# Kernel tuning notes

Measured on AMD Instinct MI355X. Metric: run time of the kernel, lower is better.

Reference implementation:

```python
import jax, jax.numpy as jnp
import numpy as np

N_SHOTS, N_SAMPLES, IMG = 10, 192, 256
M = N_SHOTS * N_SAMPLES  # 1920 k-space samples


def _radial_traj():
    # mri-nufft initialize_2D_radial: uniform spoke angles over pi,
    # radii in [-0.5, 0.5) with N_SAMPLES points per spoke.
    r = (np.arange(N_SAMPLES) - N_SAMPLES / 2) / N_SAMPLES
    ang = np.pi * np.arange(N_SHOTS) / N_SHOTS
    kx = np.cos(ang)[:, None] * r[None, :]
    ky = np.sin(ang)[:, None] * r[None, :]
    return np.stack([kx, ky], axis=-1).reshape(-1, 2).astype(np.float32)


def _phase_mats(samples):
    # Separable NDFT phase factors: exp(-2i*pi*k_x*i), exp(-2i*pi*k_y*j)
    grid = jnp.arange(IMG, dtype=jnp.float32) - IMG / 2  # centered pixel coords
    Ax = jnp.exp(-2j * jnp.pi * samples[:, 0:1] * grid[None, :]).astype(jnp.complex64)  # (M, IMG)
    Ay = jnp.exp(-2j * jnp.pi * samples[:, 1:2] * grid[None, :]).astype(jnp.complex64)  # (M, IMG)
    return Ax, Ay


def _pipe_density(samples, n_iter=10):
    # Pipe & Menon density compensation: w <- w / |F F^H w| (density=True in gpunufft).
    Ax, Ay = _phase_mats(samples)
    w = jnp.ones(M, jnp.complex64)
    for _ in range(n_iter):
        t = Ax.conj() * w[:, None]                    # (M, IMG)
        img = jnp.einsum('mi,mj->ij', t, Ay.conj())   # F^H w, (IMG, IMG)
        back = jnp.einsum('mi,ij,mj->m', Ax, img, Ay) # F F^H w, (M,)
        w = w / jnp.maximum(jnp.abs(back), 1e-12).astype(jnp.complex64)
    return jnp.abs(w).astype(jnp.float32)


def setup_inputs() -> dict:
    key = jax.random.key(0)
    k1, k2 = jax.random.split(key)
    B, C = 64, 1
    x_real = jax.random.normal(k1, (B, C, IMG, IMG), dtype=jnp.float32)
    x_imag = jax.random.normal(k2, (B, C, IMG, IMG), dtype=jnp.float32)
    samples = jnp.asarray(_radial_traj())
    density = _pipe_density(samples)
    return {"x_real": x_real, "x_imag": x_imag, "samples": samples, "density": density}


def reference(x_real, x_imag, samples, density):
    x = (x_real + 1j * x_imag).astype(jnp.complex64)  # (B, C, IMG, IMG)
    Ax, Ay = _phase_mats(samples)
    # Forward NUFFT (type-2 NDFT): kspace[b,c,m] = sum_ij Ax[m,i] Ay[m,j] x[b,c,i,j]
    t = jnp.einsum('mi,bcij->bcmj', Ax, x)            # (B, C, M, IMG)
    kspace = jnp.einsum('mj,bcmj->bcm', Ay, t)        # (B, C, M)
    # Density-compensated adjoint NUFFT (type-1 NDFT)
    kw = kspace * density.astype(jnp.complex64)
    u = jnp.einsum('mi,bcm->bcmi', Ax.conj(), kw)     # (B, C, M, IMG)
    adj = jnp.einsum('mj,bcmi->bcij', Ay.conj(), u) / (IMG * IMG)
    return jnp.stack([adj.real, adj.imag], axis=-1)   # (B, C, IMG, IMG, 2)
```

## Files before the change

### kernel.cpp

```cpp
#include <hip/hip_runtime.h>
#include <hip/hip_bf16.h>
#include <hip/hip_fp16.h>

constexpr int IMG_ = 256;
constexpr int M_   = 1920;
constexpr int B_   = 64;
constexpr int MI_  = M_ * IMG_;
constexpr int IMG2 = IMG_ * IMG_;

typedef _Float16 half8 __attribute__((ext_vector_type(8)));
typedef float    floatx4 __attribute__((ext_vector_type(4)));

__global__ __launch_bounds__(256) void phase1_k(
    const float* __restrict__ samples,
    _Float16* __restrict__ axh_r, _Float16* __restrict__ axh_i,
    _Float16* __restrict__ ayh_r, _Float16* __restrict__ ayh_i) {
  int idx = blockIdx.x * 256 + threadIdx.x;
  if (idx >= MI_) return;
  int m = idx >> 8;
  int i = idx & 255;
  float g  = (float)i - 128.0f;
  float kx = samples[2 * m + 0];
  float ky = samples[2 * m + 1];
  float sx, cx, sy, cy;
  sincospif(-2.0f * kx * g, &sx, &cx);
  sincospif(-2.0f * ky * g, &sy, &cy);
  axh_r[idx] = (_Float16)cx; axh_i[idx] = (_Float16)sx;
  ayh_r[idx] = (_Float16)cy; ayh_i[idx] = (_Float16)sy;
}

__global__ __launch_bounds__(256) void phase2_k(
    const float* __restrict__ samples,
    _Float16* __restrict__ axtc_r, _Float16* __restrict__ axtc_i,
    _Float16* __restrict__ aytc_r, _Float16* __restrict__ aytc_i) {
  int m = blockIdx.x * 256 + threadIdx.x;
  if (m >= M_) return;
  int i = blockIdx.y;
  float g  = (float)i - 128.0f;
  float kx = samples[2 * m + 0];
  float ky = samples[2 * m + 1];
  float sx, cx, sy, cy;
  sincospif(-2.0f * kx * g, &sx, &cx);
  sincospif(-2.0f * ky * g, &sy, &cy);
  int o = i * M_ + m;
  axtc_r[o] = (_Float16)cx; axtc_i[o] = (_Float16)(-sx);
  aytc_r[o] = (_Float16)cy; aytc_i[o] = (_Float16)(-sy);
}

__global__ __launch_bounds__(256) void xt_k(
    const float* __restrict__ xr, const float* __restrict__ xi,
    _Float16* __restrict__ xth_r, _Float16* __restrict__ xth_i) {
  __shared__ float tr[32][33], ti[32][33];
  const int t = threadIdx.x;
  const int b = blockIdx.z;
  const int i0 = blockIdx.x * 32, j0 = blockIdx.y * 32;
  const int r = t >> 5, c = t & 31;
#pragma unroll
  for (int k = 0; k < 4; ++k) {
    int row = r + k * 8;
    tr[row][c] = xr[(size_t)b * IMG2 + (i0 + row) * IMG_ + j0 + c];
    ti[row][c] = xi[(size_t)b * IMG2 + (i0 + row) * IMG_ + j0 + c];
  }
  __syncthreads();
#pragma unroll
  for (int k = 0; k < 4; ++k) {
    int row = r + k * 8;
    xth_r[(size_t)b * IMG2 + (j0 + row) * IMG_ + i0 + c] = (_Float16)tr[c][row];
    xth_i[(size_t)b * IMG2 + (j0 + row) * IMG_ + i0 + c] = (_Float16)ti[c][row];
  }
}

__global__ __launch_bounds__(256) void fwd_k(
    const _Float16* __restrict__ axh_r, const _Float16* __restrict__ axh_i,
    const _Float16* __restrict__ ayh_r, const _Float16* __restrict__ ayh_i,
    const _Float16* __restrict__ xth_r, const _Float16* __restrict__ xth_i,
    const float* __restrict__ density,
    _Float16* __restrict__ kwh_r, _Float16* __restrict__ kwh_i) {
  __shared__ _Float16 asr[64 * 40], asi[64 * 40];
  __shared__ _Float16 bsr[64 * 40], bsi[64 * 40];

  const int t = threadIdx.x;
  const int w = t >> 6;
  const int l = t & 63;
  const int lr = l & 15;
  const int q  = l >> 4;
  const int b  = blockIdx.y;
  const int m0 = blockIdx.x * 64;
  const _Float16* __restrict__ xrb = xth_r + (size_t)b * IMG2;
  const _Float16* __restrict__ xib = xth_i + (size_t)b * IMG2;

  float kr[4] = {0.f, 0.f, 0.f, 0.f};
  float ki[4] = {0.f, 0.f, 0.f, 0.f};
  const floatx4 z4 = {0.f, 0.f, 0.f, 0.f};

  for (int jc = 0; jc < 4; ++jc) {
    const int j0 = jc * 64;
    floatx4 accr[4] = {z4, z4, z4, z4};
    floatx4 acci[4] = {z4, z4, z4, z4};

    for (int kt = 0; kt < 8; ++kt) {
      const int i0 = kt * 32;
      __syncthreads();
#pragma unroll
      for (int p = 0; p < 2; ++p) {
        int slot = t + p * 256;
        int row = slot >> 3, seg = slot & 7;
        *(uint2*)&asr[row * 40 + seg * 4] = *(const uint2*)&axh_r[(m0 + row) * IMG_ + i0 + seg * 4];
        *(uint2*)&asi[row * 40 + seg * 4] = *(const uint2*)&axh_i[(m0 + row) * IMG_ + i0 + seg * 4];
        *(uint2*)&bsr[row * 40 + seg * 4] = *(const uint2*)&xrb[(j0 + row) * IMG_ + i0 + seg * 4];
        *(uint2*)&bsi[row * 40 + seg * 4] = *(const uint2*)&xib[(j0 + row) * IMG_ + i0 + seg * 4];
      }
      __syncthreads();

      half8 ar = *(const half8*)&asr[(w * 16 + lr) * 40 + q * 8];
      half8 ai = *(const half8*)&asi[(w * 16 + lr) * 40 + q * 8];
      half8 nai = -ai;
#pragma unroll
      for (int jt = 0; jt < 4; ++jt) {
        half8 br = *(const half8*)&bsr[(jt * 16 + lr) * 40 + q * 8];
        half8 bi = *(const half8*)&bsi[(jt * 16 + lr) * 40 + q * 8];
        accr[jt] = __builtin_amdgcn_mfma_f32_16x16x32_f16(ar,  br, accr[jt], 0, 0, 0);
        accr[jt] = __builtin_amdgcn_mfma_f32_16x16x32_f16(nai, bi, accr[jt], 0, 0, 0);
        acci[jt] = __builtin_amdgcn_mfma_f32_16x16x32_f16(ar,  bi, acci[jt], 0, 0, 0);
        acci[jt] = __builtin_amdgcn_mfma_f32_16x16x32_f16(ai,  br, acci[jt], 0, 0, 0);
      }
    }

#pragma unroll
    for (int jt = 0; jt < 4; ++jt) {
      int j = j0 + jt * 16 + lr;
#pragma unroll
      for (int reg = 0; reg < 4; ++reg) {
        int m = m0 + w * 16 + q * 4 + reg;
        float yr = (float)ayh_r[m * IMG_ + j];
        float yi = (float)ayh_i[m * IMG_ + j];
        float tr = accr[jt][reg], ti = acci[jt][reg];
        kr[reg] = fmaf(yr, tr, fmaf(-yi, ti, kr[reg]));
        ki[reg] = fmaf(yr, ti, fmaf(yi, tr, ki[reg]));
      }
    }
  }

#pragma unroll
  for (int reg = 0; reg < 4; ++reg) {
#pragma unroll
    for (int off = 1; off < 16; off <<= 1) {
      kr[reg] += __shfl_xor(kr[reg], off);
      ki[reg] += __shfl_xor(ki[reg], off);
    }
  }
  if (lr == 0) {
#pragma unroll
    for (int reg = 0; reg < 4; ++reg) {
      int m = m0 + w * 16 + q * 4 + reg;
      float d = density[m];
      kwh_r[b * M_ + m] = (_Float16)(kr[reg] * d);
      kwh_i[b * M_ + m] = (_Float16)(ki[reg] * d);
    }
  }
}

__global__ __launch_bounds__(256) void adj_k(
    const _Float16* __restrict__ axtc_r, const _Float16* __restrict__ axtc_i,
    const _Float16* __restrict__ aytc_r, const _Float16* __restrict__ aytc_i,
    const _Float16* __restrict__ kwh_r, const _Float16* __restrict__ kwh_i,
    float* __restrict__ out) {
  __shared__ _Float16 asr[64 * 40], asi[64 * 40];
  __shared__ _Float16 wsr[64 * 40], wsi[64 * 40];

  const int t = threadIdx.x;
  const int w = t >> 6;
  const int l = t & 63;
  const int lr = l & 15;
  const int q  = l >> 4;
  const int b  = blockIdx.z;
  const int i0 = blockIdx.x * 64;
  const int j0 = blockIdx.y * 64;

  const floatx4 z4 = {0.f, 0.f, 0.f, 0.f};
  floatx4 accr[4] = {z4, z4, z4, z4};
  floatx4 acci[4] = {z4, z4, z4, z4};

  for (int mt = 0; mt < M_ / 32; ++mt) {
    const int m0 = mt * 32;
    __syncthreads();
#pragma unroll
    for (int p = 0; p < 2; ++p) {
      int slot = t + p * 256;
      int row = slot >> 3, seg = slot & 7;
      *(uint2*)&asr[row * 40 + seg * 4] = *(const uint2*)&axtc_r[(i0 + row) * M_ + m0 + seg * 4];
      *(uint2*)&asi[row * 40 + seg * 4] = *(const uint2*)&axtc_i[(i0 + row) * M_ + m0 + seg * 4];
    }
    {
      int row = t >> 2, seg = t & 3;
      const __half2* ay_r = (const __half2*)&aytc_r[(j0 + row) * M_ + m0 + seg * 8];
      const __half2* ay_i = (const __half2*)&aytc_i[(j0 + row) * M_ + m0 + seg * 8];
      const __half2* kw_r = (const __half2*)&kwh_r[b * M_ + m0 + seg * 8];
      const __half2* kw_i = (const __half2*)&kwh_i[b * M_ + m0 + seg * 8];
      __half2 wr[4], wi[4];
#pragma unroll
      for (int e = 0; e < 4; ++e) {
        __half2 yr = ay_r[e], yi = ay_i[e], cr = kw_r[e], ci = kw_i[e];
        wr[e] = __hsub2(__hmul2(cr, yr), __hmul2(ci, yi));
        wi[e] = __hfma2(cr, yi, __hmul2(ci, yr));
      }
      *(uint4*)&wsr[row * 40 + seg * 8] = *(uint4*)wr;
      *(uint4*)&wsi[row * 40 + seg * 8] = *(uint4*)wi;
    }
    __syncthreads();

    half8 ar = *(const half8*)&asr[(w * 16 + lr) * 40 + q * 8];
    half8 ai = *(const half8*)&asi[(w * 16 + lr) * 40 + q * 8];
    half8 nai = -ai;
#pragma unroll
    for (int jt = 0; jt < 4; ++jt) {
      half8 br = *(const half8*)&wsr[(jt * 16 + lr) * 40 + q * 8];
      half8 bi = *(const half8*)&wsi[(jt * 16 + lr) * 40 + q * 8];
      accr[jt] = __builtin_amdgcn_mfma_f32_16x16x32_f16(ar,  br, accr[jt], 0, 0, 0);
      accr[jt] = __builtin_amdgcn_mfma_f32_16x16x32_f16(nai, bi, accr[jt], 0, 0, 0);
      acci[jt] = __builtin_amdgcn_mfma_f32_16x16x32_f16(ar,  bi, acci[jt], 0, 0, 0);
      acci[jt] = __builtin_amdgcn_mfma_f32_16x16x32_f16(ai,  br, acci[jt], 0, 0, 0);
    }
  }

  const float s = 1.0f / (float)IMG2;
#pragma unroll
  for (int jt = 0; jt < 4; ++jt) {
    int jg = j0 + jt * 16 + lr;
#pragma unroll
    for (int reg = 0; reg < 4; ++reg) {
      int ig = i0 + w * 16 + q * 4 + reg;
      float2 v = make_float2(accr[jt][reg] * s, acci[jt][reg] * s);
      *(float2*)&out[((size_t)(b * IMG_ + ig) * IMG_ + jg) * 2] = v;
    }
  }
}

extern "C" void kernel_launch(void* const* d_in, const int* in_sizes, int n_in,
                              void* d_out, int out_size, void* d_ws, size_t ws_size,
                              hipStream_t stream) {
  (void)in_sizes; (void)n_in; (void)out_size; (void)ws_size;

  const float* xr      = (const float*)d_in[0];
  const float* xi      = (const float*)d_in[1];
  const float* samples = (const float*)d_in[2];
  const float* density = (const float*)d_in[3];
  float* out = (float*)d_out;

  _Float16* f = (_Float16*)d_ws;
  _Float16* axh_r  = f + 0 * MI_;
  _Float16* axh_i  = f + 1 * MI_;
  _Float16* ayh_r  = f + 2 * MI_;
  _Float16* ayh_i  = f + 3 * MI_;
  _Float16* axtc_r = f + 4 * MI_;
  _Float16* axtc_i = f + 5 * MI_;
  _Float16* aytc_r = f + 6 * MI_;
  _Float16* aytc_i = f + 7 * MI_;
  _Float16* kwh_r  = f + 8 * MI_;
  _Float16* kwh_i  = kwh_r + B_ * M_;

  _Float16* xth_r = (_Float16*)d_out;
  _Float16* xth_i = xth_r + (size_t)B_ * IMG2;

  phase1_k<<<(MI_ + 255) / 256, 256, 0, stream>>>(samples, axh_r, axh_i, ayh_r, ayh_i);
  phase2_k<<<dim3(8, IMG_), 256, 0, stream>>>(samples, axtc_r, axtc_i, aytc_r, aytc_i);
  xt_k<<<dim3(8, 8, B_), 256, 0, stream>>>(xr, xi, xth_r, xth_i);
  fwd_k<<<dim3(M_ / 64, B_), 256, 0, stream>>>(axh_r, axh_i, ayh_r, ayh_i,
                                               xth_r, xth_i, density, kwh_r, kwh_i);
  adj_k<<<dim3(4, 4, B_), 256, 0, stream>>>(axtc_r, axtc_i, aytc_r, aytc_i,
                                            kwh_r, kwh_i, out);
}
```

Measured before the change: 288.8 us.

## Enlarge MFMA tiles to 128x128 with double-buffered direct-to-LDS loads

Both GEMM-style kernels move from a 64x64 block tile, where each wave computes a 16x64 strip, to a 128x128 tile where each wave computes 64x64 with a 4x4 accumulator grid. Operand tiles are double-buffered and fetched with global_load_lds straight into XOR-swizzled LDS, so loads for the next k-slice overlap the MFMAs on the current one. The goal is more operand reuse per LDS read, fewer global loads, and hidden memory latency. In exchange register pressure rises sharply, the grid shrinks (adj_k drops to 256 blocks, fwd_k to 960), and fwd_k now needs a cross-wave reduction through LDS.

```diff
diff --git a/kernel.cpp b/kernel.cpp
--- a/kernel.cpp
+++ b/kernel.cpp
@@ -10,6 +10,12 @@
 
 typedef _Float16 half8 __attribute__((ext_vector_type(8)));
 typedef float    floatx4 __attribute__((ext_vector_type(4)));
+
+__device__ __forceinline__ void gll16(const _Float16* g, _Float16* l) {
+  __builtin_amdgcn_global_load_lds(
+      (const __attribute__((address_space(1))) void*)g,
+      (__attribute__((address_space(3))) void*)l, 16, 0, 0);
+}
 
 __global__ __launch_bounds__(256) void phase1_k(
     const float* __restrict__ samples,
@@ -70,170 +76,278 @@
   }
 }
 
-__global__ __launch_bounds__(256) void fwd_k(
+
+__global__ __launch_bounds__(256, 2) void fwd_k(
     const _Float16* __restrict__ axh_r, const _Float16* __restrict__ axh_i,
     const _Float16* __restrict__ ayh_r, const _Float16* __restrict__ ayh_i,
     const _Float16* __restrict__ xth_r, const _Float16* __restrict__ xth_i,
     const float* __restrict__ density,
     _Float16* __restrict__ kwh_r, _Float16* __restrict__ kwh_i) {
-  __shared__ _Float16 asr[64 * 40], asi[64 * 40];
-  __shared__ _Float16 bsr[64 * 40], bsi[64 * 40];
-
-  const int t = threadIdx.x;
-  const int w = t >> 6;
-  const int l = t & 63;
+  __shared__ _Float16 lds[2][4][128 * 32];
+
+  const int t  = threadIdx.x;
+  const int w  = t >> 6;
+  const int l  = t & 63;
   const int lr = l & 15;
   const int q  = l >> 4;
+  const int wm = w >> 1;
+  const int wj = w & 1;
   const int b  = blockIdx.y;
-  const int m0 = blockIdx.x * 64;
-  const _Float16* __restrict__ xrb = xth_r + (size_t)b * IMG2;
-  const _Float16* __restrict__ xib = xth_i + (size_t)b * IMG2;
-
-  float kr[4] = {0.f, 0.f, 0.f, 0.f};
-  float ki[4] = {0.f, 0.f, 0.f, 0.f};
+  const int m0 = blockIdx.x * 128;
+
+  const int srow   = l >> 2;
+  const int schunk = (l & 3) ^ ((l >> 3) & 3);
+  const int gOffH  = srow * IMG_ + schunk * 8;
+  const int ldsWB  = (w * 16) * 32;
+  const int rc = (q ^ ((lr >> 1) & 3)) << 3;
+
   const floatx4 z4 = {0.f, 0.f, 0.f, 0.f};
-
-  for (int jc = 0; jc < 4; ++jc) {
-    const int j0 = jc * 64;
-    floatx4 accr[4] = {z4, z4, z4, z4};
-    floatx4 acci[4] = {z4, z4, z4, z4};
-
-    for (int kt = 0; kt < 8; ++kt) {
-      const int i0 = kt * 32;
-      __syncthreads();
-#pragma unroll
-      for (int p = 0; p < 2; ++p) {
-        int slot = t + p * 256;
-        int row = slot >> 3, seg = slot & 7;
-        *(uint2*)&asr[row * 40 + seg * 4] = *(const uint2*)&axh_r[(m0 + row) * IMG_ + i0 + seg * 4];
-        *(uint2*)&asi[row * 40 + seg * 4] = *(const uint2*)&axh_i[(m0 + row) * IMG_ + i0 + seg * 4];
-        *(uint2*)&bsr[row * 40 + seg * 4] = *(const uint2*)&xrb[(j0 + row) * IMG_ + i0 + seg * 4];
-        *(uint2*)&bsi[row * 40 + seg * 4] = *(const uint2*)&xib[(j0 + row) * IMG_ + i0 + seg * 4];
-      }
-      __syncthreads();
-
-      half8 ar = *(const half8*)&asr[(w * 16 + lr) * 40 + q * 8];
-      half8 ai = *(const half8*)&asi[(w * 16 + lr) * 40 + q * 8];
-      half8 nai = -ai;
+  floatx4 accr[4][4], acci[4][4];
+#pragma unroll
+  for (int a = 0; a < 4; ++a)
+#pragma unroll
+    for (int c = 0; c < 4; ++c) { accr[a][c] = z4; acci[a][c] = z4; }
+  float kr[4][4] = {}, ki[4][4] = {};
+
+  auto stage = [&](int buf, int s) {
+    const int jc = s >> 3, kt = s & 7;
+    const int col = kt * 32;
+    const size_t offA = (size_t)(m0 + w * 16) * IMG_ + col + gOffH;
+    const size_t offB = (size_t)b * IMG2 + (size_t)(jc * 128 + w * 16) * IMG_ + col + gOffH;
+    _Float16* L = &lds[buf][0][0];
+    gll16(axh_r + offA,             L + 0 * 4096 + ldsWB);
+    gll16(axh_r + offA + 64 * IMG_, L + 0 * 4096 + ldsWB + 2048);
+    gll16(axh_i + offA,             L + 1 * 4096 + ldsWB);
+    gll16(axh_i + offA + 64 * IMG_, L + 1 * 4096 + ldsWB + 2048);
+    gll16(xth_r + offB,             L + 2 * 4096 + ldsWB);
+    gll16(xth_r + offB + 64 * IMG_, L + 2 * 4096 + ldsWB + 2048);
+    gll16(xth_i + offB,             L + 3 * 4096 + ldsWB);
+    gll16(xth_i + offB + 64 * IMG_, L + 3 * 4096 + ldsWB + 2048);
+  };
+
+  auto compute = [&](int buf) {
+    const _Float16* L = &lds[buf][0][0];
+    half8 ar[4], ai[4];
+#pragma unroll
+    for (int mt = 0; mt < 4; ++mt) {
+      const int ro = (wm * 64 + mt * 16 + lr) * 32 + rc;
+      ar[mt] = *(const half8*)&L[0 * 4096 + ro];
+      ai[mt] = *(const half8*)&L[1 * 4096 + ro];
+    }
+#pragma unroll
+    for (int jt = 0; jt < 4; ++jt) {
+      const int ro = (wj * 64 + jt * 16 + lr) * 32 + rc;
+      half8 br  = *(const half8*)&L[2 * 4096 + ro];
+      half8 bi  = *(const half8*)&L[3 * 4096 + ro];
+      half8 nbi = -bi;
+#pragma unroll
+      for (int mt = 0; mt < 4; ++mt) {
+        accr[mt][jt] = __builtin_amdgcn_mfma_f32_16x16x32_f16(ar[mt], br,  accr[mt][jt], 0, 0, 0);
+        accr[mt][jt] = __builtin_amdgcn_mfma_f32_16x16x32_f16(ai[mt], nbi, accr[mt][jt], 0, 0, 0);
+        acci[mt][jt] = __builtin_amdgcn_mfma_f32_16x16x32_f16(ar[mt], bi,  acci[mt][jt], 0, 0, 0);
+        acci[mt][jt] = __builtin_amdgcn_mfma_f32_16x16x32_f16(ai[mt], br,  acci[mt][jt], 0, 0, 0);
+      }
+    }
+  };
+
+  auto epilogue = [&](int jc) {
+#pragma unroll
+    for (int mt = 0; mt < 4; ++mt)
 #pragma unroll
       for (int jt = 0; jt < 4; ++jt) {
-        half8 br = *(const half8*)&bsr[(jt * 16 + lr) * 40 + q * 8];
-        half8 bi = *(const half8*)&bsi[(jt * 16 + lr) * 40 + q * 8];
-        accr[jt] = __builtin_amdgcn_mfma_f32_16x16x32_f16(ar,  br, accr[jt], 0, 0, 0);
-        accr[jt] = __builtin_amdgcn_mfma_f32_16x16x32_f16(nai, bi, accr[jt], 0, 0, 0);
-        acci[jt] = __builtin_amdgcn_mfma_f32_16x16x32_f16(ar,  bi, acci[jt], 0, 0, 0);
-        acci[jt] = __builtin_amdgcn_mfma_f32_16x16x32_f16(ai,  br, acci[jt], 0, 0, 0);
-      }
-    }
-
-#pragma unroll
-    for (int jt = 0; jt < 4; ++jt) {
-      int j = j0 + jt * 16 + lr;
-#pragma unroll
-      for (int reg = 0; reg < 4; ++reg) {
-        int m = m0 + w * 16 + q * 4 + reg;
-        float yr = (float)ayh_r[m * IMG_ + j];
-        float yi = (float)ayh_i[m * IMG_ + j];
-        float tr = accr[jt][reg], ti = acci[jt][reg];
-        kr[reg] = fmaf(yr, tr, fmaf(-yi, ti, kr[reg]));
-        ki[reg] = fmaf(yr, ti, fmaf(yi, tr, ki[reg]));
-      }
-    }
-  }
-
-#pragma unroll
-  for (int reg = 0; reg < 4; ++reg) {
-#pragma unroll
-    for (int off = 1; off < 16; off <<= 1) {
-      kr[reg] += __shfl_xor(kr[reg], off);
-      ki[reg] += __shfl_xor(ki[reg], off);
-    }
-  }
+        const int j = jc * 128 + wj * 64 + jt * 16 + lr;
+#pragma unroll
+        for (int reg = 0; reg < 4; ++reg) {
+          const int m = m0 + wm * 64 + mt * 16 + q * 4 + reg;
+          const float yr = (float)ayh_r[m * IMG_ + j];
+          const float yi = (float)ayh_i[m * IMG_ + j];
+          const float tr = accr[mt][jt][reg], ti = acci[mt][jt][reg];
+          kr[mt][reg] = fmaf(yr, tr, fmaf(-yi, ti, kr[mt][reg]));
+          ki[mt][reg] = fmaf(yr, ti, fmaf(yi, tr, ki[mt][reg]));
+        }
+        accr[mt][jt] = z4;
+        acci[mt][jt] = z4;
+      }
+  };
+
+  stage(0, 0);
+  __syncthreads();
+  for (int s = 0; s < 16; ++s) {
+    const int buf = s & 1;
+    if (s < 15) stage(buf ^ 1, s + 1);
+    compute(buf);
+    if (s == 7)  epilogue(0);
+    if (s == 15) epilogue(1);
+    __syncthreads();
+  }
+
+#pragma unroll
+  for (int mt = 0; mt < 4; ++mt)
+#pragma unroll
+    for (int reg = 0; reg < 4; ++reg)
+#pragma unroll
+      for (int off = 1; off < 16; off <<= 1) {
+        kr[mt][reg] += __shfl_xor(kr[mt][reg], off);
+        ki[mt][reg] += __shfl_xor(ki[mt][reg], off);
+      }
+
+  float2* scr = (float2*)&lds[0][0][0];
   if (lr == 0) {
 #pragma unroll
-    for (int reg = 0; reg < 4; ++reg) {
-      int m = m0 + w * 16 + q * 4 + reg;
-      float d = density[m];
-      kwh_r[b * M_ + m] = (_Float16)(kr[reg] * d);
-      kwh_i[b * M_ + m] = (_Float16)(ki[reg] * d);
-    }
-  }
-}
-
-__global__ __launch_bounds__(256) void adj_k(
+    for (int mt = 0; mt < 4; ++mt)
+#pragma unroll
+      for (int reg = 0; reg < 4; ++reg)
+        scr[wj * 128 + wm * 64 + mt * 16 + q * 4 + reg] =
+            make_float2(kr[mt][reg], ki[mt][reg]);
+  }
+  __syncthreads();
+  if (t < 128) {
+    const int m = m0 + t;
+    const float2 p0 = scr[t], p1 = scr[128 + t];
+    const float d = density[m];
+    kwh_r[b * M_ + m] = (_Float16)((p0.x + p1.x) * d);
+    kwh_i[b * M_ + m] = (_Float16)((p0.y + p1.y) * d);
+  }
+}
+
+__global__ __launch_bounds__(256, 2) void adj_k(
     const _Float16* __restrict__ axtc_r, const _Float16* __restrict__ axtc_i,
     const _Float16* __restrict__ aytc_r, const _Float16* __restrict__ aytc_i,
     const _Float16* __restrict__ kwh_r, const _Float16* __restrict__ kwh_i,
     float* __restrict__ out) {
-  __shared__ _Float16 asr[64 * 40], asi[64 * 40];
-  __shared__ _Float16 wsr[64 * 40], wsi[64 * 40];
-
-  const int t = threadIdx.x;
-  const int w = t >> 6;
-  const int l = t & 63;
+  __shared__ _Float16 lds[2][4][128 * 32];
+
+  const int t  = threadIdx.x;
+  const int w  = t >> 6;
+  const int l  = t & 63;
   const int lr = l & 15;
   const int q  = l >> 4;
+  const int wi = w >> 1;
+  const int wj = w & 1;
   const int b  = blockIdx.z;
-  const int i0 = blockIdx.x * 64;
-  const int j0 = blockIdx.y * 64;
+  const int i0 = blockIdx.x * 128;
+  const int j0 = blockIdx.y * 128;
+
+  const int srow   = l >> 2;
+  const int schunk = (l & 3) ^ ((l >> 3) & 3);
+  const int gOffH  = srow * M_ + schunk * 8;
+  const int ldsWB  = (w * 16) * 32;
+  const int rc = (q ^ ((lr >> 1) & 3)) << 3;
+
+  const int wrow = t >> 1;
+  const int wh   = t & 1;
+  const int wp   = (wrow >> 1) & 3;
+  const int wc0  = (((2 * wh + 0) ^ wp) << 3);
+  const int wc1  = (((2 * wh + 1) ^ wp) << 3);
 
   const floatx4 z4 = {0.f, 0.f, 0.f, 0.f};
-  floatx4 accr[4] = {z4, z4, z4, z4};
-  floatx4 acci[4] = {z4, z4, z4, z4};
-
-  for (int mt = 0; mt < M_ / 32; ++mt) {
-    const int m0 = mt * 32;
+  floatx4 accr[4][4], acci[4][4];
+#pragma unroll
+  for (int a = 0; a < 4; ++a)
+#pragma unroll
+    for (int c = 0; c < 4; ++c) { accr[a][c] = z4; acci[a][c] = z4; }
+
+  uint4 Yr0, Yr1, Yi0, Yi1, Cr0, Cr1, Ci0, Ci1;
+
+  auto stageA = [&](int buf, int s) {
+    const int mc = s * 32;
+    const size_t off = (size_t)(i0 + w * 16) * M_ + mc + gOffH;
+    _Float16* L = &lds[buf][0][0];
+    gll16(axtc_r + off,           L + 0 * 4096 + ldsWB);
+    gll16(axtc_r + off + 64 * M_, L + 0 * 4096 + ldsWB + 2048);
+    gll16(axtc_i + off,           L + 1 * 4096 + ldsWB);
+    gll16(axtc_i + off + 64 * M_, L + 1 * 4096 + ldsWB + 2048);
+  };
+
+  auto loadW = [&](int s) {
+    const int mc = s * 32 + wh * 16;
+    const size_t oy = (size_t)(j0 + wrow) * M_ + mc;
+    const size_t oc = (size_t)b * M_ + mc;
+    Yr0 = *(const uint4*)&aytc_r[oy];  Yr1 = *(const uint4*)&aytc_r[oy + 8];
+    Yi0 = *(const uint4*)&aytc_i[oy];  Yi1 = *(const uint4*)&aytc_i[oy + 8];
+    Cr0 = *(const uint4*)&kwh_r[oc];   Cr1 = *(const uint4*)&kwh_r[oc + 8];
+    Ci0 = *(const uint4*)&kwh_i[oc];   Ci1 = *(const uint4*)&kwh_i[oc + 8];
+  };
+
+  auto writeW = [&](int buf) {
+    __half2 Wr0[4], Wi0[4], Wr1[4], Wi1[4];
+    {
+      const __half2* yr = (const __half2*)&Yr0; const __half2* yi = (const __half2*)&Yi0;
+      const __half2* cr = (const __half2*)&Cr0; const __half2* ci = (const __half2*)&Ci0;
+#pragma unroll
+      for (int e = 0; e < 4; ++e) {
+        Wr0[e] = __hsub2(__hmul2(cr[e], yr[e]), __hmul2(ci[e], yi[e]));
+        Wi0[e] = __hfma2(cr[e], yi[e], __hmul2(ci[e], yr[e]));
+      }
+    }
+    {
+      const __half2* yr = (const __half2*)&Yr1; const __half2* yi = (const __half2*)&Yi1;
+      const __half2* cr = (const __half2*)&Cr1; const __half2* ci = (const __half2*)&Ci1;
+#pragma unroll
+      for (int e = 0; e < 4; ++e) {
+        Wr1[e] = __hsub2(__hmul2(cr[e], yr[e]), __hmul2(ci[e], yi[e]));
+        Wi1[e] = __hfma2(cr[e], yi[e], __hmul2(ci[e], yr[e]));
+      }
+    }
+    _Float16* Lr = &lds[buf][2][0];
+    _Float16* Li = &lds[buf][3][0];
+    const int rb = wrow * 32;
+    *(uint4*)&Lr[rb + wc0] = *(const uint4*)&Wr0[0];
+    *(uint4*)&Lr[rb + wc1] = *(const uint4*)&Wr1[0];
+    *(uint4*)&Li[rb + wc0] = *(const uint4*)&Wi0[0];
+    *(uint4*)&Li[rb + wc1] = *(const uint4*)&Wi1[0];
+  };
+
+  auto compute = [&](int buf) {
+    const _Float16* L = &lds[buf][0][0];
+    half8 ar[4], ai[4];
+#pragma unroll
+    for (int mt = 0; mt < 4; ++mt) {
+      const int ro = (wi * 64 + mt * 16 + lr) * 32 + rc;
+      ar[mt] = *(const half8*)&L[0 * 4096 + ro];
+      ai[mt] = *(const half8*)&L[1 * 4096 + ro];
+    }
+#pragma unroll
+    for (int jt = 0; jt < 4; ++jt) {
+      const int ro = (wj * 64 + jt * 16 + lr) * 32 + rc;
+      half8 br  = *(const half8*)&L[2 * 4096 + ro];
+      half8 bi  = *(const half8*)&L[3 * 4096 + ro];
+      half8 nbi = -bi;
+#pragma unroll
+      for (int mt = 0; mt < 4; ++mt) {
+        accr[mt][jt] = __builtin_amdgcn_mfma_f32_16x16x32_f16(ar[mt], br,  accr[mt][jt], 0, 0, 0);
+        accr[mt][jt] = __builtin_amdgcn_mfma_f32_16x16x32_f16(ai[mt], nbi, accr[mt][jt], 0, 0, 0);
+        acci[mt][jt] = __builtin_amdgcn_mfma_f32_16x16x32_f16(ar[mt], bi,  acci[mt][jt], 0, 0, 0);
+        acci[mt][jt] = __builtin_amdgcn_mfma_f32_16x16x32_f16(ai[mt], br,  acci[mt][jt], 0, 0, 0);
+      }
+    }
+  };
+
+  loadW(0);
+  stageA(0, 0);
+  writeW(0);
+  __syncthreads();
+  for (int s = 0; s < 60; ++s) {
+    const int buf = s & 1;
+    if (s < 59) { stageA(buf ^ 1, s + 1); loadW(s + 1); }
+    compute(buf);
+    if (s < 59) writeW(buf ^ 1);
     __syncthreads();
-#pragma unroll
-    for (int p = 0; p < 2; ++p) {
-      int slot = t + p * 256;
-      int row = slot >> 3, seg = slot & 7;
-      *(uint2*)&asr[row * 40 + seg * 4] = *(const uint2*)&axtc_r[(i0 + row) * M_ + m0 + seg * 4];
-      *(uint2*)&asi[row * 40 + seg * 4] = *(const uint2*)&axtc_i[(i0 + row) * M_ + m0 + seg * 4];
-    }
-    {
-      int row = t >> 2, seg = t & 3;
-      const __half2* ay_r = (const __half2*)&aytc_r[(j0 + row) * M_ + m0 + seg * 8];
-      const __half2* ay_i = (const __half2*)&aytc_i[(j0 + row) * M_ + m0 + seg * 8];
-      const __half2* kw_r = (const __half2*)&kwh_r[b * M_ + m0 + seg * 8];
-      const __half2* kw_i = (const __half2*)&kwh_i[b * M_ + m0 + seg * 8];
-      __half2 wr[4], wi[4];
-#pragma unroll
-      for (int e = 0; e < 4; ++e) {
-        __half2 yr = ay_r[e], yi = ay_i[e], cr = kw_r[e], ci = kw_i[e];
-        wr[e] = __hsub2(__hmul2(cr, yr), __hmul2(ci, yi));
-        wi[e] = __hfma2(cr, yi, __hmul2(ci, yr));
-      }
-      *(uint4*)&wsr[row * 40 + seg * 8] = *(uint4*)wr;
-      *(uint4*)&wsi[row * 40 + seg * 8] = *(uint4*)wi;
-    }
-    __syncthreads();
-
-    half8 ar = *(const half8*)&asr[(w * 16 + lr) * 40 + q * 8];
-    half8 ai = *(const half8*)&asi[(w * 16 + lr) * 40 + q * 8];
-    half8 nai = -ai;
+  }
+
+  const float sc = 1.0f / (float)IMG2;
+#pragma unroll
+  for (int mt = 0; mt < 4; ++mt)
 #pragma unroll
     for (int jt = 0; jt < 4; ++jt) {
-      half8 br = *(const half8*)&wsr[(jt * 16 + lr) * 40 + q * 8];
-      half8 bi = *(const half8*)&wsi[(jt * 16 + lr) * 40 + q * 8];
-      accr[jt] = __builtin_amdgcn_mfma_f32_16x16x32_f16(ar,  br, accr[jt], 0, 0, 0);
-      accr[jt] = __builtin_amdgcn_mfma_f32_16x16x32_f16(nai, bi, accr[jt], 0, 0, 0);
-      acci[jt] = __builtin_amdgcn_mfma_f32_16x16x32_f16(ar,  bi, acci[jt], 0, 0, 0);
-      acci[jt] = __builtin_amdgcn_mfma_f32_16x16x32_f16(ai,  br, acci[jt], 0, 0, 0);
-    }
-  }
-
-  const float s = 1.0f / (float)IMG2;
-#pragma unroll
-  for (int jt = 0; jt < 4; ++jt) {
-    int jg = j0 + jt * 16 + lr;
-#pragma unroll
-    for (int reg = 0; reg < 4; ++reg) {
-      int ig = i0 + w * 16 + q * 4 + reg;
-      float2 v = make_float2(accr[jt][reg] * s, acci[jt][reg] * s);
-      *(float2*)&out[((size_t)(b * IMG_ + ig) * IMG_ + jg) * 2] = v;
-    }
-  }
+      const int jg = j0 + wj * 64 + jt * 16 + lr;
+#pragma unroll
+      for (int reg = 0; reg < 4; ++reg) {
+        const int ig = i0 + wi * 64 + mt * 16 + q * 4 + reg;
+        float2 v = make_float2(accr[mt][jt][reg] * sc, acci[mt][jt][reg] * sc);
+        *(float2*)&out[((size_t)(b * IMG_ + ig) * IMG_ + jg) * 2] = v;
+      }
+    }
 }
 
 extern "C" void kernel_launch(void* const* d_in, const int* in_sizes, int n_in,
@@ -265,8 +379,8 @@
   phase1_k<<<(MI_ + 255) / 256, 256, 0, stream>>>(samples, axh_r, axh_i, ayh_r, ayh_i);
   phase2_k<<<dim3(8, IMG_), 256, 0, stream>>>(samples, axtc_r, axtc_i, aytc_r, aytc_i);
   xt_k<<<dim3(8, 8, B_), 256, 0, stream>>>(xr, xi, xth_r, xth_i);
-  fwd_k<<<dim3(M_ / 64, B_), 256, 0, stream>>>(axh_r, axh_i, ayh_r, ayh_i,
-                                               xth_r, xth_i, density, kwh_r, kwh_i);
-  adj_k<<<dim3(4, 4, B_), 256, 0, stream>>>(axtc_r, axtc_i, aytc_r, aytc_i,
+  fwd_k<<<dim3(M_ / 128, B_), 256, 0, stream>>>(axh_r, axh_i, ayh_r, ayh_i,
+                                                xth_r, xth_i, density, kwh_r, kwh_i);
+  adj_k<<<dim3(2, 2, B_), 256, 0, stream>>>(axtc_r, axtc_i, aytc_r, aytc_i,
                                             kwh_r, kwh_i, out);
 }
```

Measured after the change: 620.6 us. 115% more time.
